# Kernel tuning notes

Hardware: AMD Instinct MI355X
Metric: run time of the kernel (lower is better)

## Reference

```python
import jax, jax.numpy as jnp
import numpy as np

BN_EPS = 1e-5

def _bn(x, g, b, m, v):
    # eval-mode BatchNorm1d with running stats
    return (x - m) * jax.lax.rsqrt(v + BN_EPS) * g + b

def _gcn(h, src, dst, norm, W, b, N):
    # PyG GCNConv: out[dst] += norm * (h @ W)[src]; then add bias
    msg = (h @ W)[src] * norm[:, None]
    return jax.ops.segment_sum(msg, dst, num_segments=N) + b

def setup_inputs() -> dict:
    key = jax.random.key(0)
    ks = jax.random.split(key, 24)
    N, E, F = 300000, 3000000, 25
    d = {}
    d['x'] = jax.random.normal(ks[0], (N, F), jnp.float32)
    d['edge_index'] = jax.random.randint(ks[1], (2, E), 0, N, dtype=jnp.int64)
    def lin(k, i, o):
        return jax.random.normal(k, (i, o), jnp.float32) / np.float32(np.sqrt(i))
    # ffn1: Linear(25,100) -> BN(100) -> ReLU -> Dropout -> Linear(100,25) -> BN(25) -> Dropout
    d['W1'] = lin(ks[2], 25, 100); d['b1'] = jnp.zeros((100,), jnp.float32)
    d['g1'] = jnp.ones((100,), jnp.float32); d['beta1'] = jnp.zeros((100,), jnp.float32)
    d['m1'] = jnp.zeros((100,), jnp.float32); d['v1'] = jnp.ones((100,), jnp.float32)
    d['W2'] = lin(ks[3], 100, 25); d['b2'] = jnp.zeros((25,), jnp.float32)
    d['g2'] = jnp.ones((25,), jnp.float32); d['beta2'] = jnp.zeros((25,), jnp.float32)
    d['m2'] = jnp.zeros((25,), jnp.float32); d['v2'] = jnp.ones((25,), jnp.float32)
    # GCN layers actually used in forward
    d['Wc1'] = lin(ks[4], 25, 25); d['bc1'] = jnp.zeros((25,), jnp.float32)
    d['Wc2'] = lin(ks[5], 25, 16); d['bc2'] = jnp.zeros((16,), jnp.float32)
    d['Wc3'] = lin(ks[6], 16, 16); d['bc3'] = jnp.zeros((16,), jnp.float32)
    d['Wc4'] = lin(ks[7], 16, 8);  d['bc4'] = jnp.zeros((8,), jnp.float32)
    d['Wc5'] = lin(ks[8], 8, 4);   d['bc5'] = jnp.zeros((4,), jnp.float32)
    # fc: reshape yields 1200 cols (source's Linear(4800,4) is a bug; use 1200)
    d['Wfc'] = lin(ks[9], 1200, 4); d['bfc'] = jnp.zeros((4,), jnp.float32)
    return d

def reference(x, edge_index, W1, b1, g1, beta1, m1, v1, W2, b2, g2, beta2, m2, v2,
              Wc1, bc1, Wc2, bc2, Wc3, bc3, Wc4, bc4, Wc5, bc5, Wfc, bfc):
    N = x.shape[0]
    # add self-loops and compute symmetric normalization once (shared graph)
    loops = jnp.arange(N, dtype=edge_index.dtype)
    src = jnp.concatenate([edge_index[0], loops])
    dst = jnp.concatenate([edge_index[1], loops])
    deg = jax.ops.segment_sum(jnp.ones_like(dst, jnp.float32), dst, num_segments=N)
    dinv = jnp.where(deg > 0, jax.lax.rsqrt(deg), 0.0)
    norm = dinv[src] * dinv[dst]
    # ffn1 (eval mode: dropout is identity)
    h = _bn(x @ W1 + b1, g1, beta1, m1, v1)
    h = jax.nn.relu(h)
    h = _bn(h @ W2 + b2, g2, beta2, m2, v2)
    # stacked GCN layers
    h = jax.nn.relu(_gcn(h, src, dst, norm, Wc1, bc1, N))
    h = jax.nn.relu(_gcn(h, src, dst, norm, Wc2, bc2, N))
    h = jax.nn.relu(_gcn(h, src, dst, norm, Wc3, bc3, N))
    h = jax.nn.relu(_gcn(h, src, dst, norm, Wc4, bc4, N))
    h = jax.nn.relu(_gcn(h, src, dst, norm, Wc5, bc5, N))
    h = h.reshape(-1, 300 * 4)  # [N/300, 1200]
    return h @ Wfc + bfc
```

## Files before the change

### kernel.cpp

```cpp
#include <hip/hip_runtime.h>

#define BN_EPS 1e-5f
#define ELLW 48
#define BSH2 11
#define NPB 2048
#define MAXBK 160
#define BCAP2 26624

__global__ void k_detect(const unsigned int* __restrict__ ei, int* __restrict__ flag) {
    int t = threadIdx.x;
    unsigned int v = ei[2 * t + 1];
    unsigned long long mask = __ballot(v != 0);
    if (t == 0) flag[0] = (mask == 0ULL) ? 1 : 0;
}

__global__ __launch_bounds__(256) void k_part(
    const int* __restrict__ ei, const int* __restrict__ flag,
    int* __restrict__ gcnt, int* __restrict__ bdata, int E)
{
    __shared__ int hist[MAXBK];
    __shared__ int cur[MAXBK];
    __shared__ int gbase[MAXBK];
    __shared__ int locstart[MAXBK + 1];
    __shared__ int sc[256];
    __shared__ int stage[1024];

    int t = threadIdx.x;
    int blockBase = blockIdx.x * 1024;
    int blockCnt = E - blockBase; if (blockCnt > 1024) blockCnt = 1024; if (blockCnt < 0) blockCnt = 0;

    for (int i = t; i < MAXBK; i += 256) hist[i] = 0;
    __syncthreads();

    bool w64 = (flag[0] != 0);
    int e = blockBase + t * 4;
    int s[4], d[4];
    int cnt = 0;
    if (e < E) {
        cnt = E - e; if (cnt > 4) cnt = 4;
        if (cnt == 4) {
            if (w64) {
                const int4* ps = (const int4*)(ei + (size_t)2 * e);
                int4 a = ps[0], b = ps[1];
                s[0] = a.x; s[1] = a.z; s[2] = b.x; s[3] = b.z;
                const int4* pd = (const int4*)(ei + (size_t)2 * ((size_t)E + e));
                int4 c = pd[0], f = pd[1];
                d[0] = c.x; d[1] = c.z; d[2] = f.x; d[3] = f.z;
            } else {
                int4 a = *(const int4*)(ei + e);
                s[0] = a.x; s[1] = a.y; s[2] = a.z; s[3] = a.w;
                int4 c = *(const int4*)(ei + (size_t)E + e);
                d[0] = c.x; d[1] = c.y; d[2] = c.z; d[3] = c.w;
            }
        } else {
            for (int i = 0; i < cnt; ++i) {
                if (w64) { s[i] = ei[(size_t)2 * (e + i)]; d[i] = ei[(size_t)2 * ((size_t)E + e + i)]; }
                else     { s[i] = ei[e + i];               d[i] = ei[(size_t)E + e + i]; }
            }
        }
    }
    int bk[4], pk[4];
    for (int i = 0; i < cnt; ++i) {
        bk[i] = d[i] >> BSH2;
        pk[i] = (s[i] << BSH2) | (d[i] & (NPB - 1));
        atomicAdd(&hist[bk[i]], 1);
    }
    __syncthreads();

    sc[t] = (t < MAXBK) ? hist[t] : 0;
    __syncthreads();
    for (int off = 1; off < 256; off <<= 1) {
        int x = (t >= off) ? sc[t - off] : 0;
        __syncthreads();
        sc[t] += x;
        __syncthreads();
    }
    if (t < MAXBK) {
        locstart[t] = sc[t] - hist[t];
        cur[t] = sc[t] - hist[t];
        if (hist[t] > 0) gbase[t] = atomicAdd(&gcnt[t], hist[t]);
    }
    if (t == 255) locstart[MAXBK] = sc[MAXBK - 1];
    __syncthreads();

    for (int i = 0; i < cnt; ++i) {
        int p = atomicAdd(&cur[bk[i]], 1);
        stage[p] = pk[i];
    }
    __syncthreads();

    for (int sIdx = t; sIdx < blockCnt; sIdx += 256) {
        int lo = 0, hi = MAXBK;
        while (hi - lo > 1) {
            int mid = (lo + hi) >> 1;
            if (locstart[mid] <= sIdx) lo = mid; else hi = mid;
        }
        int g = gbase[lo] + (sIdx - locstart[lo]);
        if (g < BCAP2) bdata[(size_t)lo * BCAP2 + g] = stage[sIdx];
    }
}

__global__ __launch_bounds__(256) void k_ell2(
    const int* __restrict__ gcnt, const int* __restrict__ bdata,
    int* __restrict__ ell, float* __restrict__ dinv, int N)
{
    __shared__ int lcnt[NPB];
    int b = blockIdx.x;
    int t = threadIdx.x;
    for (int i = t; i < NPB; i += 256) lcnt[i] = 0;
    __syncthreads();
    int base = b << BSH2;
    int cnt = min(gcnt[b], BCAP2);
    const int* __restrict__ bd = bdata + (size_t)b * BCAP2;
    for (int i = t; i < cnt; i += 256) {
        int v = bd[i];
        int dl = v & (NPB - 1);
        int src = v >> BSH2;
        int pos = atomicAdd(&lcnt[dl], 1);
        if (pos < ELLW - 4)
            ell[(size_t)(base + dl) * ELLW + 4 + pos] = src;
    }
    __syncthreads();
    for (int i = t; i < NPB; i += 256) {
        int n = base + i;
        if (n < N) {
            int c = lcnt[i];
            ell[(size_t)n * ELLW] = c;
            dinv[n] = 1.0f / sqrtf((float)(c + 1));
        }
    }
}

__global__ __launch_bounds__(256) void k_prep(
    const float* __restrict__ W1, const float* __restrict__ b1,
    const float* __restrict__ g1, const float* __restrict__ be1,
    const float* __restrict__ m1, const float* __restrict__ v1,
    const float* __restrict__ W2, const float* __restrict__ b2,
    const float* __restrict__ g2, const float* __restrict__ be2,
    const float* __restrict__ m2, const float* __restrict__ v2,
    const float* __restrict__ Wc1, float* __restrict__ prep)
{
    __shared__ float s1[100], bb1[100], s2[25], bb2[25], wc[625];
    int t = threadIdx.x;
    if (t < 100) {
        float s = g1[t] * rsqrtf(v1[t] + BN_EPS);
        s1[t] = s; bb1[t] = (b1[t] - m1[t]) * s + be1[t];
    }
    if (t >= 128 && t < 153) {
        int u = t - 128;
        float s = g2[u] * rsqrtf(v2[u] + BN_EPS);
        s2[u] = s; bb2[u] = (b2[u] - m2[u]) * s + be2[u];
    }
    for (int q = t; q < 625; q += 256) wc[q] = Wc1[q];
    __syncthreads();
    for (int q = t; q < 2500; q += 256) {
        int kc = q / 625, r = q % 625;
        int j = r / 25, kk = r % 25;
        int k = kc * 25 + kk;
        prep[q] = W1[j * 100 + k] * s1[k];
    }
    for (int q = t; q < 2500; q += 256) {
        int kc = q / 625, r = q % 625;
        int kk = r / 25, j = r % 25;
        int k = kc * 25 + kk;
        float acc = 0.0f;
        for (int m = 0; m < 25; ++m) acc += W2[k * 25 + m] * s2[m] * wc[m * 25 + j];
        prep[2500 + q] = acc;
    }
    if (t < 100) prep[5000 + t] = bb1[t];
    if (t >= 128 && t < 153) {
        int j = t - 128;
        float acc = 0.0f;
        for (int m = 0; m < 25; ++m) acc += bb2[m] * wc[m * 25 + j];
        prep[5104 + j] = acc;
    }
}

__global__ __launch_bounds__(256, 4) void k_ffn(
    const float* __restrict__ prep, const float* __restrict__ x,
    const float* __restrict__ dinv, float* __restrict__ T, int N)
{
    int n = blockIdx.x * 256 + threadIdx.x;
    if (n >= N) return;

    float xi[25];
#pragma unroll
    for (int j = 0; j < 25; ++j) xi[j] = x[(size_t)n * 25 + j];

    float o[25];
#pragma unroll
    for (int j = 0; j < 25; ++j) o[j] = 0.0f;

#pragma unroll 1
    for (int kc = 0; kc < 4; ++kc) {
        const float* __restrict__ w1c = prep + kc * 625;
        const float* __restrict__ w2c = prep + 2500 + kc * 625;
        const float* __restrict__ b1c = prep + 5000 + kc * 25;
        float hm[25];
#pragma unroll
        for (int kk = 0; kk < 25; ++kk) hm[kk] = b1c[kk];
#pragma unroll
        for (int j = 0; j < 25; ++j) {
            float xv = xi[j];
#pragma unroll
            for (int kk = 0; kk < 25; ++kk) hm[kk] += xv * w1c[j * 25 + kk];
        }
#pragma unroll
        for (int kk = 0; kk < 25; ++kk) {
            float r = fmaxf(hm[kk], 0.0f);
#pragma unroll
            for (int j = 0; j < 25; ++j) o[j] += r * w2c[kk * 25 + j];
        }
    }

    float dv = dinv[n];
    float o32[32];
#pragma unroll
    for (int j = 0; j < 25; ++j) o32[j] = (o[j] + prep[5104 + j]) * dv;
#pragma unroll
    for (int j = 25; j < 32; ++j) o32[j] = 0.0f;
    float4* T4 = (float4*)(T + (size_t)n * 32);
#pragma unroll
    for (int q = 0; q < 8; ++q)
        T4[q] = make_float4(o32[4 * q], o32[4 * q + 1], o32[4 * q + 2], o32[4 * q + 3]);
}

template <int DI, int SI, int DO, int LPN>
__global__ __launch_bounds__(256) void k_layer(
    const int* __restrict__ ell,
    const float* __restrict__ dinv, const float* __restrict__ bias,
    const float* __restrict__ W,
    const float* __restrict__ Tin, float* __restrict__ Tout, int N)
{
    constexpr int SI4 = SI / 4;
    constexpr int DO4 = DO / 4;
    constexpr int PAD = LPN * 4;
    __shared__ float sW[DI * DO];
    __shared__ float sB[PAD];
    int t = threadIdx.x;
    for (int i = t; i < DI * DO; i += 256) sW[i] = W[i];
    for (int i = t; i < PAD; i += 256) sB[i] = (i < DI) ? bias[i] : 0.0f;
    __syncthreads();

    int g = t / LPN;
    int j = t % LPN;
    int n = blockIdx.x * (256 / LPN) + g;
    int nc = (n < N) ? n : (N - 1);
    const int* __restrict__ row = ell + (size_t)nc * ELLW;
    int dg = min(row[0], ELLW - 4);
    if (n >= N) dg = 0;
    float dv = dinv[nc];
    const float4* __restrict__ T4 = (const float4*)Tin;

    float4 a0 = T4[(size_t)nc * SI4 + j];
    float4 a1 = make_float4(0.f, 0.f, 0.f, 0.f);
    float4 a2 = a1, a3 = a1;
    const int4* __restrict__ rowv = (const int4*)(row + 4);
    int k = 0;
    for (; k + 3 < dg; k += 4) {
        int4 s4 = rowv[k >> 2];
        float4 v0 = T4[(size_t)s4.x * SI4 + j];
        float4 v1 = T4[(size_t)s4.y * SI4 + j];
        float4 v2 = T4[(size_t)s4.z * SI4 + j];
        float4 v3 = T4[(size_t)s4.w * SI4 + j];
        a0.x += v0.x; a0.y += v0.y; a0.z += v0.z; a0.w += v0.w;
        a1.x += v1.x; a1.y += v1.y; a1.z += v1.z; a1.w += v1.w;
        a2.x += v2.x; a2.y += v2.y; a2.z += v2.z; a2.w += v2.w;
        a3.x += v3.x; a3.y += v3.y; a3.z += v3.z; a3.w += v3.w;
    }
    for (; k < dg; ++k) {
        float4 v = T4[(size_t)row[4 + k] * SI4 + j];
        a0.x += v.x; a0.y += v.y; a0.z += v.z; a0.w += v.w;
    }
    float ar[4];
    ar[0] = fmaxf(dv * (a0.x + a1.x + a2.x + a3.x) + sB[4 * j + 0], 0.0f);
    ar[1] = fmaxf(dv * (a0.y + a1.y + a2.y + a3.y) + sB[4 * j + 1], 0.0f);
    ar[2] = fmaxf(dv * (a0.z + a1.z + a2.z + a3.z) + sB[4 * j + 2], 0.0f);
    ar[3] = fmaxf(dv * (a0.w + a1.w + a2.w + a3.w) + sB[4 * j + 3], 0.0f);

    int lane = t & 63;
    int base = lane - j;
    int jo = (j < DO4) ? j : 0;
    const float4* __restrict__ sW4 = (const float4*)sW;
    float4 o = make_float4(0.f, 0.f, 0.f, 0.f);
#pragma unroll
    for (int k2 = 0; k2 < DI; ++k2) {
        float av = __shfl(ar[k2 & 3], base + (k2 >> 2));
        float4 w = sW4[k2 * DO4 + jo];
        o.x += av * w.x; o.y += av * w.y; o.z += av * w.z; o.w += av * w.w;
    }
    if (n < N && j < DO4)
        ((float4*)Tout)[(size_t)n * DO4 + j] =
            make_float4(dv * o.x, dv * o.y, dv * o.z, dv * o.w);
}

__global__ __launch_bounds__(256) void k_final(
    const int* __restrict__ ell,
    const float* __restrict__ dinv, const float* __restrict__ bias,
    const float* __restrict__ Tin, float* __restrict__ Tout, int N)
{
    int n = blockIdx.x * 256 + threadIdx.x;
    if (n >= N) return;
    const int* __restrict__ row = ell + (size_t)n * ELLW;
    int dg = min(row[0], ELLW - 4);
    float dv = dinv[n];
    const float4* __restrict__ T4 = (const float4*)Tin;

    float4 a0 = T4[n];
    float4 a1 = make_float4(0.f, 0.f, 0.f, 0.f);
    float4 a2 = a1, a3 = a1;
    const int4* __restrict__ rowv = (const int4*)(row + 4);
    int k = 0;
    for (; k + 3 < dg; k += 4) {
        int4 s4 = rowv[k >> 2];
        float4 v0 = T4[s4.x], v1 = T4[s4.y], v2 = T4[s4.z], v3 = T4[s4.w];
        a0.x += v0.x; a0.y += v0.y; a0.z += v0.z; a0.w += v0.w;
        a1.x += v1.x; a1.y += v1.y; a1.z += v1.z; a1.w += v1.w;
        a2.x += v2.x; a2.y += v2.y; a2.z += v2.z; a2.w += v2.w;
        a3.x += v3.x; a3.y += v3.y; a3.z += v3.z; a3.w += v3.w;
    }
    for (; k < dg; ++k) {
        float4 v = T4[row[4 + k]];
        a0.x += v.x; a0.y += v.y; a0.z += v.z; a0.w += v.w;
    }
    float4 b = *(const float4*)bias;
    ((float4*)Tout)[n] = make_float4(
        fmaxf(dv * (a0.x + a1.x + a2.x + a3.x) + b.x, 0.0f),
        fmaxf(dv * (a0.y + a1.y + a2.y + a3.y) + b.y, 0.0f),
        fmaxf(dv * (a0.z + a1.z + a2.z + a3.z) + b.z, 0.0f),
        fmaxf(dv * (a0.w + a1.w + a2.w + a3.w) + b.w, 0.0f));
}

__global__ __launch_bounds__(256) void k_fc(
    const float* __restrict__ H, const float* __restrict__ Wfc,
    const float* __restrict__ bfc, float* __restrict__ out)
{
    int r = blockIdx.x;
    int t = threadIdx.x;
    float p0 = 0.f, p1 = 0.f, p2 = 0.f, p3 = 0.f;
    for (int k = t; k < 1200; k += 256) {
        float h = H[(size_t)r * 1200 + k];
        p0 += h * Wfc[k * 4 + 0];
        p1 += h * Wfc[k * 4 + 1];
        p2 += h * Wfc[k * 4 + 2];
        p3 += h * Wfc[k * 4 + 3];
    }
#pragma unroll
    for (int off = 32; off > 0; off >>= 1) {
        p0 += __shfl_down(p0, off);
        p1 += __shfl_down(p1, off);
        p2 += __shfl_down(p2, off);
        p3 += __shfl_down(p3, off);
    }
    __shared__ float red[4][4];
    int w = t >> 6, lane = t & 63;
    if (lane == 0) { red[w][0] = p0; red[w][1] = p1; red[w][2] = p2; red[w][3] = p3; }
    __syncthreads();
    if (t < 4) {
        float s = red[0][t] + red[1][t] + red[2][t] + red[3][t];
        out[r * 4 + t] = s + bfc[t];
    }
}

extern "C" void kernel_launch(void* const* d_in, const int* in_sizes, int n_in,
                              void* d_out, int out_size, void* d_ws, size_t ws_size,
                              hipStream_t stream) {
    const float* x   = (const float*)d_in[0];
    const int*   ei  = (const int*)d_in[1];
    const float* W1  = (const float*)d_in[2];
    const float* b1  = (const float*)d_in[3];
    const float* g1  = (const float*)d_in[4];
    const float* be1 = (const float*)d_in[5];
    const float* m1  = (const float*)d_in[6];
    const float* v1  = (const float*)d_in[7];
    const float* W2  = (const float*)d_in[8];
    const float* b2  = (const float*)d_in[9];
    const float* g2  = (const float*)d_in[10];
    const float* be2 = (const float*)d_in[11];
    const float* m2  = (const float*)d_in[12];
    const float* v2  = (const float*)d_in[13];
    const float* Wc1 = (const float*)d_in[14];
    const float* bc1 = (const float*)d_in[15];
    const float* Wc2 = (const float*)d_in[16];
    const float* bc2 = (const float*)d_in[17];
    const float* Wc3 = (const float*)d_in[18];
    const float* bc3 = (const float*)d_in[19];
    const float* Wc4 = (const float*)d_in[20];
    const float* bc4 = (const float*)d_in[21];
    const float* Wc5 = (const float*)d_in[22];
    const float* bc5 = (const float*)d_in[23];
    const float* Wfc = (const float*)d_in[24];
    const float* bfc = (const float*)d_in[25];

    const int N = in_sizes[0] / 25;
    const int E = in_sizes[1] / 2;
    const int NBUCK = (N + NPB - 1) >> BSH2;

    char* ws = (char*)d_ws;
    size_t off = 0;
    auto alloc = [&](size_t bytes) { size_t o = off; off += (bytes + 255) & ~(size_t)255; return o; };
    size_t o_flag = alloc(256);
    size_t o_gcnt = alloc((size_t)MAXBK * 4);
    size_t o_prep = alloc(6144 * 4);
    size_t o_dinv = alloc((size_t)N * 4);
    size_t o_ell  = alloc((size_t)N * ELLW * 4);
    size_t o_A = alloc((size_t)N * 32 * 4);
    size_t o_B = alloc((size_t)N * 16 * 4);
    (void)alloc(4096);

    int*   flag = (int*)(ws + o_flag);
    int*   gcnt = (int*)(ws + o_gcnt);
    float* prep = (float*)(ws + o_prep);
    float* dinv = (float*)(ws + o_dinv);
    int*   ell  = (int*)(ws + o_ell);
    float* A = (float*)(ws + o_A);
    float* B_ = (float*)(ws + o_B);
    int*   bdata = (int*)A;

    const int B = 256;
    int gN = (N + B - 1) / B;
    int gP = (E + 1023) / 1024;

    k_detect<<<1, 64, 0, stream>>>((const unsigned int*)ei, flag);
    hipMemsetAsync(gcnt, 0, (size_t)MAXBK * 4, stream);
    k_prep<<<1, B, 0, stream>>>(W1, b1, g1, be1, m1, v1, W2, b2, g2, be2, m2, v2, Wc1, prep);
    k_part<<<gP, B, 0, stream>>>(ei, flag, gcnt, bdata, E);
    k_ell2<<<NBUCK, B, 0, stream>>>(gcnt, bdata, ell, dinv, N);

    k_ffn<<<gN, B, 0, stream>>>(prep, x, dinv, A, N);
    k_layer<25, 32, 16, 8><<<(N * 8 + B - 1) / B, B, 0, stream>>>(ell, dinv, bc1, Wc2, A, B_, N);
    k_layer<16, 16, 16, 4><<<(N * 4 + B - 1) / B, B, 0, stream>>>(ell, dinv, bc2, Wc3, B_, A, N);
    k_layer<16, 16, 8, 4><<<(N * 4 + B - 1) / B, B, 0, stream>>>(ell, dinv, bc3, Wc4, A, B_, N);
    k_layer<8, 8, 4, 2><<<(N * 2 + B - 1) / B, B, 0, stream>>>(ell, dinv, bc4, Wc5, B_, A, N);
    k_final<<<gN, B, 0, stream>>>(ell, dinv, bc5, A, B_, N);
    k_fc<<<1000, B, 0, stream>>>(B_, Wfc, bfc, (float*)d_out);
}
```

Baseline: 529.5 us.

## Fuse FFN with edge partitioning and defer source dinv scaling to first layer

Merges k_detect, the gcnt memset and k_prep into one two-block setup kernel. It also fuses the FFN and the edge-bucketing partition into one launch, so that dense FFN blocks and scatter blocks run concurrently instead of serially. Because the FFN no longer depends on dinv, it drops the dinv multiply and the first GCN layer instead gathers dinv[src] for each neighbor. That adds an extra gathered load per edge in that layer. The gather loops also prefetch the next int4 of neighbor indices, and bdata moves to buffer B so it does not overlap the FFN output.

```diff
diff --git a/kernel.cpp b/kernel.cpp
--- a/kernel.cpp
+++ b/kernel.cpp
@@ -7,96 +7,198 @@
 #define MAXBK 160
 #define BCAP2 26624
 
-__global__ void k_detect(const unsigned int* __restrict__ ei, int* __restrict__ flag) {
+struct PartS {
+    int hist[MAXBK];
+    int cur[MAXBK];
+    int gbase[MAXBK];
+    int locstart[MAXBK + 1];
+    int sc[256];
+    int stage[1024];
+};
+
+__global__ __launch_bounds__(256) void k_setup(
+    const float* __restrict__ W1, const float* __restrict__ b1,
+    const float* __restrict__ g1, const float* __restrict__ be1,
+    const float* __restrict__ m1, const float* __restrict__ v1,
+    const float* __restrict__ W2, const float* __restrict__ b2,
+    const float* __restrict__ g2, const float* __restrict__ be2,
+    const float* __restrict__ m2, const float* __restrict__ v2,
+    const float* __restrict__ Wc1, float* __restrict__ prep,
+    const unsigned int* __restrict__ ei2, int* __restrict__ flag,
+    int* __restrict__ gcnt)
+{
     int t = threadIdx.x;
-    unsigned int v = ei[2 * t + 1];
-    unsigned long long mask = __ballot(v != 0);
-    if (t == 0) flag[0] = (mask == 0ULL) ? 1 : 0;
-}
-
-__global__ __launch_bounds__(256) void k_part(
+    if (blockIdx.x == 1) {
+        if (t < MAXBK) gcnt[t] = 0;
+        if (t < 64) {
+            unsigned int v = ei2[2 * t + 1];
+            unsigned long long mask = __ballot(v != 0);
+            if (t == 0) flag[0] = (mask == 0ULL) ? 1 : 0;
+        }
+        return;
+    }
+    __shared__ float s1[100], bb1[100], s2[25], bb2[25], wc[625];
+    if (t < 100) {
+        float s = g1[t] * rsqrtf(v1[t] + BN_EPS);
+        s1[t] = s; bb1[t] = (b1[t] - m1[t]) * s + be1[t];
+    }
+    if (t >= 128 && t < 153) {
+        int u = t - 128;
+        float s = g2[u] * rsqrtf(v2[u] + BN_EPS);
+        s2[u] = s; bb2[u] = (b2[u] - m2[u]) * s + be2[u];
+    }
+    for (int q = t; q < 625; q += 256) wc[q] = Wc1[q];
+    __syncthreads();
+    for (int q = t; q < 2500; q += 256) {
+        int kc = q / 625, r = q % 625;
+        int j = r / 25, kk = r % 25;
+        int k = kc * 25 + kk;
+        prep[q] = W1[j * 100 + k] * s1[k];
+    }
+    for (int q = t; q < 2500; q += 256) {
+        int kc = q / 625, r = q % 625;
+        int kk = r / 25, j = r % 25;
+        int k = kc * 25 + kk;
+        float acc = 0.0f;
+        for (int m = 0; m < 25; ++m) acc += W2[k * 25 + m] * s2[m] * wc[m * 25 + j];
+        prep[2500 + q] = acc;
+    }
+    if (t < 100) prep[5000 + t] = bb1[t];
+    if (t >= 128 && t < 153) {
+        int j = t - 128;
+        float acc = 0.0f;
+        for (int m = 0; m < 25; ++m) acc += bb2[m] * wc[m * 25 + j];
+        prep[5104 + j] = acc;
+    }
+}
+
+__global__ __launch_bounds__(256, 4) void k_ffnpart(
+    const float* __restrict__ prep, const float* __restrict__ x,
+    float* __restrict__ T,
     const int* __restrict__ ei, const int* __restrict__ flag,
-    int* __restrict__ gcnt, int* __restrict__ bdata, int E)
-{
-    __shared__ int hist[MAXBK];
-    __shared__ int cur[MAXBK];
-    __shared__ int gbase[MAXBK];
-    __shared__ int locstart[MAXBK + 1];
-    __shared__ int sc[256];
-    __shared__ int stage[1024];
-
+    int* __restrict__ gcnt, int* __restrict__ bdata,
+    int nFfn, int N, int E)
+{
+    __shared__ char smem_raw[sizeof(PartS)];
     int t = threadIdx.x;
-    int blockBase = blockIdx.x * 1024;
-    int blockCnt = E - blockBase; if (blockCnt > 1024) blockCnt = 1024; if (blockCnt < 0) blockCnt = 0;
-
-    for (int i = t; i < MAXBK; i += 256) hist[i] = 0;
-    __syncthreads();
-
-    bool w64 = (flag[0] != 0);
-    int e = blockBase + t * 4;
-    int s[4], d[4];
-    int cnt = 0;
-    if (e < E) {
-        cnt = E - e; if (cnt > 4) cnt = 4;
-        if (cnt == 4) {
-            if (w64) {
-                const int4* ps = (const int4*)(ei + (size_t)2 * e);
-                int4 a = ps[0], b = ps[1];
-                s[0] = a.x; s[1] = a.z; s[2] = b.x; s[3] = b.z;
-                const int4* pd = (const int4*)(ei + (size_t)2 * ((size_t)E + e));
-                int4 c = pd[0], f = pd[1];
-                d[0] = c.x; d[1] = c.z; d[2] = f.x; d[3] = f.z;
+
+    if ((int)blockIdx.x < nFfn) {
+        int n = (int)blockIdx.x * 256 + t;
+        if (n >= N) return;
+
+        float xi[25];
+#pragma unroll
+        for (int j = 0; j < 25; ++j) xi[j] = x[(size_t)n * 25 + j];
+
+        float o[25];
+#pragma unroll
+        for (int j = 0; j < 25; ++j) o[j] = 0.0f;
+
+#pragma unroll 1
+        for (int kc = 0; kc < 4; ++kc) {
+            const float* __restrict__ w1c = prep + kc * 625;
+            const float* __restrict__ w2c = prep + 2500 + kc * 625;
+            const float* __restrict__ b1c = prep + 5000 + kc * 25;
+            float hm[25];
+#pragma unroll
+            for (int kk = 0; kk < 25; ++kk) hm[kk] = b1c[kk];
+#pragma unroll
+            for (int j = 0; j < 25; ++j) {
+                float xv = xi[j];
+#pragma unroll
+                for (int kk = 0; kk < 25; ++kk) hm[kk] += xv * w1c[j * 25 + kk];
+            }
+#pragma unroll
+            for (int kk = 0; kk < 25; ++kk) {
+                float r = fmaxf(hm[kk], 0.0f);
+#pragma unroll
+                for (int j = 0; j < 25; ++j) o[j] += r * w2c[kk * 25 + j];
+            }
+        }
+
+        float o32[32];
+#pragma unroll
+        for (int j = 0; j < 25; ++j) o32[j] = o[j] + prep[5104 + j];
+#pragma unroll
+        for (int j = 25; j < 32; ++j) o32[j] = 0.0f;
+        float4* T4 = (float4*)(T + (size_t)n * 32);
+#pragma unroll
+        for (int q = 0; q < 8; ++q)
+            T4[q] = make_float4(o32[4 * q], o32[4 * q + 1], o32[4 * q + 2], o32[4 * q + 3]);
+    } else {
+        PartS& S = *reinterpret_cast<PartS*>(smem_raw);
+        int blockBase = ((int)blockIdx.x - nFfn) * 1024;
+        int blockCnt = E - blockBase; if (blockCnt > 1024) blockCnt = 1024; if (blockCnt < 0) blockCnt = 0;
+
+        for (int i = t; i < MAXBK; i += 256) S.hist[i] = 0;
+        __syncthreads();
+
+        bool w64 = (flag[0] != 0);
+        int e = blockBase + t * 4;
+        int s[4], d[4];
+        int cnt = 0;
+        if (e < E) {
+            cnt = E - e; if (cnt > 4) cnt = 4;
+            if (cnt == 4) {
+                if (w64) {
+                    const int4* ps = (const int4*)(ei + (size_t)2 * e);
+                    int4 a = ps[0], b = ps[1];
+                    s[0] = a.x; s[1] = a.z; s[2] = b.x; s[3] = b.z;
+                    const int4* pd = (const int4*)(ei + (size_t)2 * ((size_t)E + e));
+                    int4 c = pd[0], f = pd[1];
+                    d[0] = c.x; d[1] = c.z; d[2] = f.x; d[3] = f.z;
+                } else {
+                    int4 a = *(const int4*)(ei + e);
+                    s[0] = a.x; s[1] = a.y; s[2] = a.z; s[3] = a.w;
+                    int4 c = *(const int4*)(ei + (size_t)E + e);
+                    d[0] = c.x; d[1] = c.y; d[2] = c.z; d[3] = c.w;
+                }
             } else {
-                int4 a = *(const int4*)(ei + e);
-                s[0] = a.x; s[1] = a.y; s[2] = a.z; s[3] = a.w;
-                int4 c = *(const int4*)(ei + (size_t)E + e);
-                d[0] = c.x; d[1] = c.y; d[2] = c.z; d[3] = c.w;
+                for (int i = 0; i < cnt; ++i) {
+                    if (w64) { s[i] = ei[(size_t)2 * (e + i)]; d[i] = ei[(size_t)2 * ((size_t)E + e + i)]; }
+                    else     { s[i] = ei[e + i];               d[i] = ei[(size_t)E + e + i]; }
+                }
             }
-        } else {
-            for (int i = 0; i < cnt; ++i) {
-                if (w64) { s[i] = ei[(size_t)2 * (e + i)]; d[i] = ei[(size_t)2 * ((size_t)E + e + i)]; }
-                else     { s[i] = ei[e + i];               d[i] = ei[(size_t)E + e + i]; }
+        }
+        int bk[4], pk[4];
+        for (int i = 0; i < cnt; ++i) {
+            bk[i] = d[i] >> BSH2;
+            pk[i] = (s[i] << BSH2) | (d[i] & (NPB - 1));
+            atomicAdd(&S.hist[bk[i]], 1);
+        }
+        __syncthreads();
+
+        S.sc[t] = (t < MAXBK) ? S.hist[t] : 0;
+        __syncthreads();
+        for (int off = 1; off < 256; off <<= 1) {
+            int xv = (t >= off) ? S.sc[t - off] : 0;
+            __syncthreads();
+            S.sc[t] += xv;
+            __syncthreads();
+        }
+        if (t < MAXBK) {
+            S.locstart[t] = S.sc[t] - S.hist[t];
+            S.cur[t] = S.sc[t] - S.hist[t];
+            if (S.hist[t] > 0) S.gbase[t] = atomicAdd(&gcnt[t], S.hist[t]);
+        }
+        if (t == 255) S.locstart[MAXBK] = S.sc[MAXBK - 1];
+        __syncthreads();
+
+        for (int i = 0; i < cnt; ++i) {
+            int p = atomicAdd(&S.cur[bk[i]], 1);
+            S.stage[p] = pk[i];
+        }
+        __syncthreads();
+
+        for (int sIdx = t; sIdx < blockCnt; sIdx += 256) {
+            int lo = 0, hi = MAXBK;
+            while (hi - lo > 1) {
+                int mid = (lo + hi) >> 1;
+                if (S.locstart[mid] <= sIdx) lo = mid; else hi = mid;
             }
-        }
-    }
-    int bk[4], pk[4];
-    for (int i = 0; i < cnt; ++i) {
-        bk[i] = d[i] >> BSH2;
-        pk[i] = (s[i] << BSH2) | (d[i] & (NPB - 1));
-        atomicAdd(&hist[bk[i]], 1);
-    }
-    __syncthreads();
-
-    sc[t] = (t < MAXBK) ? hist[t] : 0;
-    __syncthreads();
-    for (int off = 1; off < 256; off <<= 1) {
-        int x = (t >= off) ? sc[t - off] : 0;
-        __syncthreads();
-        sc[t] += x;
-        __syncthreads();
-    }
-    if (t < MAXBK) {
-        locstart[t] = sc[t] - hist[t];
-        cur[t] = sc[t] - hist[t];
-        if (hist[t] > 0) gbase[t] = atomicAdd(&gcnt[t], hist[t]);
-    }
-    if (t == 255) locstart[MAXBK] = sc[MAXBK - 1];
-    __syncthreads();
-
-    for (int i = 0; i < cnt; ++i) {
-        int p = atomicAdd(&cur[bk[i]], 1);
-        stage[p] = pk[i];
-    }
-    __syncthreads();
-
-    for (int sIdx = t; sIdx < blockCnt; sIdx += 256) {
-        int lo = 0, hi = MAXBK;
-        while (hi - lo > 1) {
-            int mid = (lo + hi) >> 1;
-            if (locstart[mid] <= sIdx) lo = mid; else hi = mid;
-        }
-        int g = gbase[lo] + (sIdx - locstart[lo]);
-        if (g < BCAP2) bdata[(size_t)lo * BCAP2 + g] = stage[sIdx];
+            int gp = S.gbase[lo] + (sIdx - S.locstart[lo]);
+            if (gp < BCAP2) bdata[(size_t)lo * BCAP2 + gp] = S.stage[sIdx];
+        }
     }
 }
 
@@ -131,101 +233,7 @@
     }
 }
 
-__global__ __launch_bounds__(256) void k_prep(
-    const float* __restrict__ W1, const float* __restrict__ b1,
-    const float* __restrict__ g1, const float* __restrict__ be1,
-    const float* __restrict__ m1, const float* __restrict__ v1,
-    const float* __restrict__ W2, const float* __restrict__ b2,
-    const float* __restrict__ g2, const float* __restrict__ be2,
-    const float* __restrict__ m2, const float* __restrict__ v2,
-    const float* __restrict__ Wc1, float* __restrict__ prep)
-{
-    __shared__ float s1[100], bb1[100], s2[25], bb2[25], wc[625];
-    int t = threadIdx.x;
-    if (t < 100) {
-        float s = g1[t] * rsqrtf(v1[t] + BN_EPS);
-        s1[t] = s; bb1[t] = (b1[t] - m1[t]) * s + be1[t];
-    }
-    if (t >= 128 && t < 153) {
-        int u = t - 128;
-        float s = g2[u] * rsqrtf(v2[u] + BN_EPS);
-        s2[u] = s; bb2[u] = (b2[u] - m2[u]) * s + be2[u];
-    }
-    for (int q = t; q < 625; q += 256) wc[q] = Wc1[q];
-    __syncthreads();
-    for (int q = t; q < 2500; q += 256) {
-        int kc = q / 625, r = q % 625;
-        int j = r / 25, kk = r % 25;
-        int k = kc * 25 + kk;
-        prep[q] = W1[j * 100 + k] * s1[k];
-    }
-    for (int q = t; q < 2500; q += 256) {
-        int kc = q / 625, r = q % 625;
-        int kk = r / 25, j = r % 25;
-        int k = kc * 25 + kk;
-        float acc = 0.0f;
-        for (int m = 0; m < 25; ++m) acc += W2[k * 25 + m] * s2[m] * wc[m * 25 + j];
-        prep[2500 + q] = acc;
-    }
-    if (t < 100) prep[5000 + t] = bb1[t];
-    if (t >= 128 && t < 153) {
-        int j = t - 128;
-        float acc = 0.0f;
-        for (int m = 0; m < 25; ++m) acc += bb2[m] * wc[m * 25 + j];
-        prep[5104 + j] = acc;
-    }
-}
-
-__global__ __launch_bounds__(256, 4) void k_ffn(
-    const float* __restrict__ prep, const float* __restrict__ x,
-    const float* __restrict__ dinv, float* __restrict__ T, int N)
-{
-    int n = blockIdx.x * 256 + threadIdx.x;
-    if (n >= N) return;
-
-    float xi[25];
-#pragma unroll
-    for (int j = 0; j < 25; ++j) xi[j] = x[(size_t)n * 25 + j];
-
-    float o[25];
-#pragma unroll
-    for (int j = 0; j < 25; ++j) o[j] = 0.0f;
-
-#pragma unroll 1
-    for (int kc = 0; kc < 4; ++kc) {
-        const float* __restrict__ w1c = prep + kc * 625;
-        const float* __restrict__ w2c = prep + 2500 + kc * 625;
-        const float* __restrict__ b1c = prep + 5000 + kc * 25;
-        float hm[25];
-#pragma unroll
-        for (int kk = 0; kk < 25; ++kk) hm[kk] = b1c[kk];
-#pragma unroll
-        for (int j = 0; j < 25; ++j) {
-            float xv = xi[j];
-#pragma unroll
-            for (int kk = 0; kk < 25; ++kk) hm[kk] += xv * w1c[j * 25 + kk];
-        }
-#pragma unroll
-        for (int kk = 0; kk < 25; ++kk) {
-            float r = fmaxf(hm[kk], 0.0f);
-#pragma unroll
-            for (int j = 0; j < 25; ++j) o[j] += r * w2c[kk * 25 + j];
-        }
-    }
-
-    float dv = dinv[n];
-    float o32[32];
-#pragma unroll
-    for (int j = 0; j < 25; ++j) o32[j] = (o[j] + prep[5104 + j]) * dv;
-#pragma unroll
-    for (int j = 25; j < 32; ++j) o32[j] = 0.0f;
-    float4* T4 = (float4*)(T + (size_t)n * 32);
-#pragma unroll
-    for (int q = 0; q < 8; ++q)
-        T4[q] = make_float4(o32[4 * q], o32[4 * q + 1], o32[4 * q + 2], o32[4 * q + 3]);
-}
-
-template <int DI, int SI, int DO, int LPN>
+template <int DI, int SI, int DO, int LPN, bool SDV>
 __global__ __launch_bounds__(256) void k_layer(
     const int* __restrict__ ell,
     const float* __restrict__ dinv, const float* __restrict__ bias,
@@ -253,24 +261,40 @@
     const float4* __restrict__ T4 = (const float4*)Tin;
 
     float4 a0 = T4[(size_t)nc * SI4 + j];
+    if (SDV) { a0.x *= dv; a0.y *= dv; a0.z *= dv; a0.w *= dv; }
     float4 a1 = make_float4(0.f, 0.f, 0.f, 0.f);
     float4 a2 = a1, a3 = a1;
     const int4* __restrict__ rowv = (const int4*)(row + 4);
     int k = 0;
+    int4 s4;
+    if (k + 3 < dg) s4 = rowv[0];
     for (; k + 3 < dg; k += 4) {
-        int4 s4 = rowv[k >> 2];
+        bool more = (k + 7 < dg);
+        int4 nx;
+        if (more) nx = rowv[(k >> 2) + 1];
         float4 v0 = T4[(size_t)s4.x * SI4 + j];
         float4 v1 = T4[(size_t)s4.y * SI4 + j];
         float4 v2 = T4[(size_t)s4.z * SI4 + j];
         float4 v3 = T4[(size_t)s4.w * SI4 + j];
-        a0.x += v0.x; a0.y += v0.y; a0.z += v0.z; a0.w += v0.w;
-        a1.x += v1.x; a1.y += v1.y; a1.z += v1.z; a1.w += v1.w;
-        a2.x += v2.x; a2.y += v2.y; a2.z += v2.z; a2.w += v2.w;
-        a3.x += v3.x; a3.y += v3.y; a3.z += v3.z; a3.w += v3.w;
+        if (SDV) {
+            float d0 = dinv[s4.x], d1 = dinv[s4.y], d2 = dinv[s4.z], d3 = dinv[s4.w];
+            a0.x += d0 * v0.x; a0.y += d0 * v0.y; a0.z += d0 * v0.z; a0.w += d0 * v0.w;
+            a1.x += d1 * v1.x; a1.y += d1 * v1.y; a1.z += d1 * v1.z; a1.w += d1 * v1.w;
+            a2.x += d2 * v2.x; a2.y += d2 * v2.y; a2.z += d2 * v2.z; a2.w += d2 * v2.w;
+            a3.x += d3 * v3.x; a3.y += d3 * v3.y; a3.z += d3 * v3.z; a3.w += d3 * v3.w;
+        } else {
+            a0.x += v0.x; a0.y += v0.y; a0.z += v0.z; a0.w += v0.w;
+            a1.x += v1.x; a1.y += v1.y; a1.z += v1.z; a1.w += v1.w;
+            a2.x += v2.x; a2.y += v2.y; a2.z += v2.z; a2.w += v2.w;
+            a3.x += v3.x; a3.y += v3.y; a3.z += v3.z; a3.w += v3.w;
+        }
+        if (more) s4 = nx;
     }
     for (; k < dg; ++k) {
-        float4 v = T4[(size_t)row[4 + k] * SI4 + j];
-        a0.x += v.x; a0.y += v.y; a0.z += v.z; a0.w += v.w;
+        int sidx = row[4 + k];
+        float4 v = T4[(size_t)sidx * SI4 + j];
+        float dd = SDV ? dinv[sidx] : 1.0f;
+        a0.x += dd * v.x; a0.y += dd * v.y; a0.z += dd * v.z; a0.w += dd * v.w;
     }
     float ar[4];
     ar[0] = fmaxf(dv * (a0.x + a1.x + a2.x + a3.x) + sB[4 * j + 0], 0.0f);
@@ -311,13 +335,18 @@
     float4 a2 = a1, a3 = a1;
     const int4* __restrict__ rowv = (const int4*)(row + 4);
     int k = 0;
+    int4 s4;
+    if (k + 3 < dg) s4 = rowv[0];
     for (; k + 3 < dg; k += 4) {
-        int4 s4 = rowv[k >> 2];
+        bool more = (k + 7 < dg);
+        int4 nx;
+        if (more) nx = rowv[(k >> 2) + 1];
         float4 v0 = T4[s4.x], v1 = T4[s4.y], v2 = T4[s4.z], v3 = T4[s4.w];
         a0.x += v0.x; a0.y += v0.y; a0.z += v0.z; a0.w += v0.w;
         a1.x += v1.x; a1.y += v1.y; a1.z += v1.z; a1.w += v1.w;
         a2.x += v2.x; a2.y += v2.y; a2.z += v2.z; a2.w += v2.w;
         a3.x += v3.x; a3.y += v3.y; a3.z += v3.z; a3.w += v3.w;
+        if (more) s4 = nx;
     }
     for (; k < dg; ++k) {
         float4 v = T4[row[4 + k]];
@@ -415,23 +444,22 @@
     int*   ell  = (int*)(ws + o_ell);
     float* A = (float*)(ws + o_A);
     float* B_ = (float*)(ws + o_B);
-    int*   bdata = (int*)A;
+    int*   bdata = (int*)B_;
 
     const int B = 256;
     int gN = (N + B - 1) / B;
+    int gF = gN;
     int gP = (E + 1023) / 1024;
 
-    k_detect<<<1, 64, 0, stream>>>((const unsigned int*)ei, flag);
-    hipMemsetAsync(gcnt, 0, (size_t)MAXBK * 4, stream);
-    k_prep<<<1, B, 0, stream>>>(W1, b1, g1, be1, m1, v1, W2, b2, g2, be2, m2, v2, Wc1, prep);
-    k_part<<<gP, B, 0, stream>>>(ei, flag, gcnt, bdata, E);
+    k_setup<<<2, B, 0, stream>>>(W1, b1, g1, be1, m1, v1, W2, b2, g2, be2, m2, v2,
+                                 Wc1, prep, (const unsigned int*)ei, flag, gcnt);
+    k_ffnpart<<<gF + gP, B, 0, stream>>>(prep, x, A, ei, flag, gcnt, bdata, gF, N, E);
     k_ell2<<<NBUCK, B, 0, stream>>>(gcnt, bdata, ell, dinv, N);
 
-    k_ffn<<<gN, B, 0, stream>>>(prep, x, dinv, A, N);
-    k_layer<25, 32, 16, 8><<<(N * 8 + B - 1) / B, B, 0, stream>>>(ell, dinv, bc1, Wc2, A, B_, N);
-    k_layer<16, 16, 16, 4><<<(N * 4 + B - 1) / B, B, 0, stream>>>(ell, dinv, bc2, Wc3, B_, A, N);
-    k_layer<16, 16, 8, 4><<<(N * 4 + B - 1) / B, B, 0, stream>>>(ell, dinv, bc3, Wc4, A, B_, N);
-    k_layer<8, 8, 4, 2><<<(N * 2 + B - 1) / B, B, 0, stream>>>(ell, dinv, bc4, Wc5, B_, A, N);
+    k_layer<25, 32, 16, 8, true><<<(N * 8 + B - 1) / B, B, 0, stream>>>(ell, dinv, bc1, Wc2, A, B_, N);
+    k_layer<16, 16, 16, 4, false><<<(N * 4 + B - 1) / B, B, 0, stream>>>(ell, dinv, bc2, Wc3, B_, A, N);
+    k_layer<16, 16, 8, 4, false><<<(N * 4 + B - 1) / B, B, 0, stream>>>(ell, dinv, bc3, Wc4, A, B_, N);
+    k_layer<8, 8, 4, 2, false><<<(N * 2 + B - 1) / B, B, 0, stream>>>(ell, dinv, bc4, Wc5, B_, A, N);
     k_final<<<gN, B, 0, stream>>>(ell, dinv, bc5, A, B_, N);
     k_fc<<<1000, B, 0, stream>>>(B_, Wfc, bfc, (float*)d_out);
 }
```

Result: faster. 480.5 us (-9.2%).
